# Kernel optimization log

Hardware: AMD Instinct MI355X
Metric: run time of the kernel (lower is better)

## Reference

```python
import jax, jax.numpy as jnp
import numpy as np

ALPHA = 0.1
B, T, D = 32, 1024, 384


def _build_alive(T):
    # Expert j (1-indexed) is created at time j with lifetime 2^(ctz(j)+2)+1.
    def lifetime(j):
        k = (j & -j).bit_length() - 1
        return 2 ** (k + 2) + 1

    sets = [[j for j in range(1, t + 1) if t < j + lifetime(j)]
            for t in range(1, T + 1)]
    K = max(len(s) for s in sets)
    # pad with sentinel index T (the extra never-consumed expert slot)
    idx = np.full((T, K), T, dtype=np.int32)
    mask = np.zeros((T, K), dtype=np.float32)
    for t0, s in enumerate(sets):
        for i, j in enumerate(s):
            idx[t0, i] = j - 1  # 0-indexed expert slot
            mask[t0, i] = 1.0
    return idx, mask


def setup_inputs() -> dict:
    key = jax.random.key(0)
    kx, kw, kb = jax.random.split(key, 3)
    n_exp = T + 1
    x = jax.random.normal(kx, (B, T, D), dtype=jnp.float32)
    # stand-in STULayer = Linear(D, D) per expert
    W = jax.random.normal(kw, (n_exp, D, D), dtype=jnp.float32) / np.float32(np.sqrt(D))
    b = jax.random.normal(kb, (n_exp, D), dtype=jnp.float32) * 0.02
    idx, mask = _build_alive(T)
    return {"x": x, "W": W, "b": b,
            "alive_idx": jnp.asarray(idx), "alive_mask": jnp.asarray(mask)}


def reference(x, W, b, alive_idx, alive_mask):
    Bb, Tt, Dd = x.shape
    n_exp = W.shape[0]
    # initial pool: 1 expert with weight 1
    p0 = jnp.zeros((n_exp,), x.dtype).at[0].set(1.0)
    new_idx = jnp.arange(1, Tt + 1, dtype=jnp.int32)      # slot of expert created at step t
    t_f = jnp.arange(1, Tt + 1, dtype=x.dtype)            # p[new] = 1/t

    def step(p, inp):
        x_t, idx, mask, ni, tf = inp          # x_t: [B,D]; idx,mask: [K]
        Wg = W[idx]                            # [K,D,D]
        bg = b[idx]                            # [K,D]
        outs = jnp.einsum('bd,kde->kbe', x_t, Wg) + bg[:, None, :]  # [K,B,D]
        p_a = p[idx] * mask                    # weights of alive experts
        w = p_a / jnp.sum(p_a)                 # normalized (torch keeps them pre-normalized)
        y_t = jnp.einsum('k,kbe->be', w, outs)
        # soft cross-entropy of expert outputs against x_t (ChunkedCrossEntropyLoss stand-in)
        tgt = jax.nn.softmax(x_t, axis=-1)                       # [B,D]
        logp = jax.nn.log_softmax(outs, axis=-1)                 # [K,B,D]
        loss = -jnp.mean(jnp.sum(tgt[None, :, :] * logp, axis=-1), axis=-1)  # [K]
        loss = jax.lax.stop_gradient(loss)     # torch uses .item() => detached
        # multiplicative weight update, normalize over alive set
        p_upd = p_a * jnp.exp(-ALPHA * loss) * mask
        p_upd = p_upd / jnp.sum(p_upd)
        p = p.at[idx].set(jnp.where(mask > 0, p_upd, p[idx]))
        # spawn new expert with weight 1/t (renormalization deferred to use time)
        p = p.at[ni].set(1.0 / tf)
        return p, y_t

    xs = (jnp.swapaxes(x, 0, 1), alive_idx, alive_mask, new_idx, t_f)
    _, ys = jax.lax.scan(step, p0, xs)        # ys: [T,B,D]
    return jnp.swapaxes(ys, 0, 1)
```

## Files before the change

### kernel.cpp

```cpp
#include <hip/hip_runtime.h>

#define TT 1024
#define BB 32
#define DD 384
#define NE 1025
#define ALPHA_ 0.1f
#define TC 4
#define KSTEP 64
#define NKS 6
#define MROWS 128
#define PADK 72
#define NTHR 512

typedef __attribute__((ext_vector_type(8))) short short8;
typedef __attribute__((ext_vector_type(8))) unsigned short ushort8;
typedef __attribute__((ext_vector_type(4))) float f32x4;

__device__ __forceinline__ unsigned short f2bf(float f) {
    unsigned int u = __float_as_uint(f);
    unsigned int r = u + 0x7fffu + ((u >> 16) & 1u);
    return (unsigned short)(r >> 16);
}

__device__ __host__ __forceinline__ int chunks_of(int j, int* Lout) {
    int k = __builtin_ctz(j);
    int life = (1 << (k + 2)) + 1;
    int jend = j + life - 1; if (jend > TT) jend = TT;
    int L = jend - j + 1;
    *Lout = L;
    return (L + TC - 1) / TC;
}

__device__ __forceinline__ void gl16(const void* g, void* l) {
    __builtin_amdgcn_global_load_lds(
        (const __attribute__((address_space(1))) void*)g,
        (__attribute__((address_space(3))) void*)l, 16, 0, 0);
}

__device__ __forceinline__ float dppsum32(float v) {
    float t;
    t = __int_as_float(__builtin_amdgcn_update_dpp(0, __float_as_int(v), 0x111, 0xf, 0xf, true)); v += t;
    t = __int_as_float(__builtin_amdgcn_update_dpp(0, __float_as_int(v), 0x112, 0xf, 0xf, true)); v += t;
    t = __int_as_float(__builtin_amdgcn_update_dpp(0, __float_as_int(v), 0x114, 0xf, 0xf, true)); v += t;
    t = __int_as_float(__builtin_amdgcn_update_dpp(0, __float_as_int(v), 0x118, 0xf, 0xf, true)); v += t;
    t = __int_as_float(__builtin_amdgcn_update_dpp(0, __float_as_int(v), 0x142, 0xf, 0xf, true)); v += t;
    return __int_as_float(__builtin_amdgcn_readlane(__float_as_int(v), 31));
}

__global__ void setup_blocks(int* __restrict__ table) {
    int j = threadIdx.x + 1;
    int L; int nc = chunks_of(j, &L);
    int start = 0;
    for (int jp = 1; jp < j; ++jp) { int Lp; start += chunks_of(jp, &Lp); }
    for (int c = 0; c < nc; ++c) {
        int cnt = L - c * TC; if (cnt > TC) cnt = TC;
        int* e = table + 3 * (start + c);
        e[0] = j - 1;
        e[1] = (j - 1) + c * TC;
        e[2] = cnt;
    }
}

__global__ void setup_pref(const float* __restrict__ amask, int* __restrict__ pref, int K) {
    __shared__ int sc[1024];
    int t = threadIdx.x;
    int c = 0;
    for (int kk = 0; kk < K; ++kk) c += (amask[t * K + kk] > 0.f) ? 1 : 0;
    sc[t] = c;
    __syncthreads();
    for (int off = 1; off < 1024; off <<= 1) {
        int v = (t >= off) ? sc[t - off] : 0;
        __syncthreads();
        sc[t] += v;
        __syncthreads();
    }
    if (t == 0) pref[0] = 0;
    pref[t + 1] = sc[t];
}

__global__ void setup_union(int* __restrict__ uCount, int* __restrict__ uList) {
    int c = threadIdx.x;
    int t1 = 2 * c + 1, t2 = 2 * c + 2;
    int n = 0;
    for (int j = 1; j <= t2 && j <= TT; ++j) {
        int k = __builtin_ctz(j);
        int life = (1 << (k + 2)) + 1;
        if (j + life - 1 >= t1) { if (n < 32) uList[c * 32 + n] = j - 1; n++; }
    }
    uCount[c] = n > 32 ? 32 : n;
}

__global__ void setup_perm3(const int* __restrict__ aidx, const float* __restrict__ amask,
                            short* __restrict__ perm16, int K) {
    int t0 = blockIdx.x;
    int l = threadIdx.x;
    short enc = 63;
    if (t0 >= 1 && t0 <= TT - 1 && l < K && amask[t0 * K + l] > 0.f) {
        int sp = aidx[t0 * K + l];
        if (sp == t0) enc = (short)(-sp);
        else {
            for (int kk = 0; kk < K; ++kk)
                if (aidx[(t0 - 1) * K + kk] == sp) { enc = (short)kk; break; }
        }
    }
    perm16[t0 * 32 + l] = enc;
}

__global__ void conv_w(const float* __restrict__ W, unsigned short* __restrict__ Wperm) {
    int db = blockIdx.x;
    int j  = blockIdx.y;
    __shared__ __align__(16) unsigned short sL[12288];
    int tid = threadIdx.x;
    int r = tid >> 4, q = tid & 15;
    const float* src = W + (size_t)j * (DD * DD) + (size_t)(db * 32 + r) * DD + q * 24;
#pragma unroll
    for (int i = 0; i < 6; ++i) {
        float4 f = *(const float4*)(src + i * 4);
        int e0 = q * 24 + i * 4;
        float fv[4] = {f.x, f.y, f.z, f.w};
#pragma unroll
        for (int m = 0; m < 4; ++m) {
            int e = e0 + m;
            int off = (e >> 4) * 512 + (r >> 3) * 128 + (e & 15) * 8 + (r & 7);
            sL[off] = f2bf(fv[m]);
        }
    }
    __syncthreads();
    ushort8* dst = (ushort8*)(Wperm + ((size_t)j * 12 + db) * 12288);
    const ushort8* s8 = (const ushort8*)sL;
#pragma unroll
    for (int i = 0; i < 3; ++i) dst[tid * 3 + i] = s8[tid * 3 + i];
}

__global__ void conv_x(const float* __restrict__ x, unsigned short* __restrict__ xperm) {
    int t = blockIdx.x;
    __shared__ __align__(16) unsigned short sL[12288];
    int tid = threadIdx.x;
    int b = tid >> 4, q = tid & 15;
    const float* src = x + ((size_t)b * TT + t) * DD + q * 24;
#pragma unroll
    for (int i = 0; i < 6; ++i) {
        float4 f = *(const float4*)(src + i * 4);
        int d0 = q * 24 + i * 4;
        float fv[4] = {f.x, f.y, f.z, f.w};
#pragma unroll
        for (int m = 0; m < 4; ++m) {
            int d = d0 + m;
            int off = ((b >> 4) * 12 + (d >> 5)) * 512 + ((d >> 3) & 3) * 128 + (b & 15) * 8 + (d & 7);
            sL[off] = f2bf(fv[m]);
        }
    }
    __syncthreads();
    ushort8* dst = (ushort8*)(xperm + (size_t)t * 12288);
    const ushort8* s8 = (const ushort8*)sL;
#pragma unroll
    for (int i = 0; i < 3; ++i) dst[tid * 3 + i] = s8[tid * 3 + i];
}

__global__ void conv_tgt(const float* __restrict__ x, unsigned short* __restrict__ tgtbf) {
    __shared__ unsigned short sL[8 * 384];
    int tid = threadIdx.x;
    int wid = tid >> 6, lane = tid & 63;
    size_t row = (size_t)blockIdx.x * 8 + wid;
    const float* xr = x + row * DD;
    float v[6]; float m = -1e30f;
#pragma unroll
    for (int i = 0; i < 6; ++i) { v[i] = xr[lane + 64 * i]; m = fmaxf(m, v[i]); }
#pragma unroll
    for (int d = 1; d < 64; d <<= 1) m = fmaxf(m, __shfl_xor(m, d));
    float s = 0.f;
#pragma unroll
    for (int i = 0; i < 6; ++i) { v[i] = __expf(v[i] - m); s += v[i]; }
#pragma unroll
    for (int d = 1; d < 64; d <<= 1) s += __shfl_xor(s, d);
    float rz = 1.0f / s;
#pragma unroll
    for (int i = 0; i < 6; ++i) sL[wid * 384 + lane + 64 * i] = f2bf(v[i] * rz);
    __syncthreads();
    unsigned int* dst = (unsigned int*)(tgtbf + (size_t)blockIdx.x * 8 * 384);
    const unsigned int* s32 = (const unsigned int*)sL;
#pragma unroll
    for (int i = 0; i < 3; ++i) dst[tid * 3 + i] = s32[tid * 3 + i];
}

__global__ __launch_bounds__(1024)
void gemmA(const unsigned short* __restrict__ xperm,
           const unsigned short* __restrict__ Wperm,
           const float* __restrict__ bias,
           const int* __restrict__ aidx,
           const unsigned short* __restrict__ tgtbf,
           float* __restrict__ Epad,
           const int* __restrict__ table, int nblk, int K,
           const int* __restrict__ pref,
           unsigned short* __restrict__ outs)
{
    __shared__ __align__(16) unsigned short sA[2][4096];
    __shared__ __align__(16) unsigned short sB[2][12288];
    __shared__ float sRow[128];
    __shared__ int sKK[TC];
    __shared__ int sSlot[TC];

    int bid = blockIdx.x;
    int q8 = nblk >> 3, r8 = nblk & 7;
    int xcd = bid & 7, pos = bid >> 3;
    int lb = (xcd < r8 ? xcd * (q8 + 1) : r8 * (q8 + 1) + (xcd - r8) * q8) + pos;

    int s = table[3 * lb], t0s = table[3 * lb + 1], cnt = table[3 * lb + 2];

    int tid = threadIdx.x;
    int wid = tid >> 6, lane = tid & 63;
    int waveM = wid >> 2, waveN = wid & 3;
    int lc = lane & 15, lg = lane >> 4;

    int tcl[4];
#pragma unroll
    for (int tc = 0; tc < 4; ++tc) { int t = t0s + tc; tcl[tc] = t > TT - 1 ? TT - 1 : t; }

    f32x4 acc[2][6];
    f32x4 zz = {0.f, 0.f, 0.f, 0.f};
#pragma unroll
    for (int m = 0; m < 2; ++m)
#pragma unroll
        for (int n = 0; n < 6; ++n) acc[m][n] = zz;

    const size_t wbase = (size_t)s * (12 * 24 * 512);

    auto stage = [&](int buf, int ks) {
        if (wid < 8) {
            int tc = wid >> 1, bb = wid & 1;
            const unsigned short* asrc = xperm + ((size_t)tcl[tc] * 24 + bb * 12 + ks) * 512 + lane * 8;
            gl16(asrc, &sA[buf][wid * 512]);
            const unsigned short* bsrc = Wperm + wbase + ((size_t)ks * 24 + 16 + wid) * 512 + lane * 8;
            gl16(bsrc, &sB[buf][(16 + wid) * 512]);
        } else {
            int e0 = (wid - 8) * 2;
            const unsigned short* b0 = Wperm + wbase + ((size_t)ks * 24 + e0) * 512 + lane * 8;
            gl16(b0, &sB[buf][e0 * 512]);
            gl16(b0 + 512, &sB[buf][(e0 + 1) * 512]);
        }
    };

    stage(0, 0);
    __syncthreads();
    for (int ks = 0; ks < 12; ++ks) {
        int cur = ks & 1;
        if (ks < 11) stage(cur ^ 1, ks + 1);
        short8 af[2], bfr[6];
#pragma unroll
        for (int mf = 0; mf < 2; ++mf)
            af[mf] = *(const short8*)&sA[cur][(waveM * 2 + mf) * 512 + lane * 8];
#pragma unroll
        for (int nf = 0; nf < 6; ++nf)
            bfr[nf] = *(const short8*)&sB[cur][(waveN * 6 + nf) * 512 + lane * 8];
#pragma unroll
        for (int mf = 0; mf < 2; ++mf)
#pragma unroll
            for (int nf = 0; nf < 6; ++nf)
                acc[mf][nf] = __builtin_amdgcn_mfma_f32_16x16x32_bf16(af[mf], bfr[nf], acc[mf][nf], 0, 0, 0);
        __syncthreads();
    }

    float* sStat = (float*)&sA[0][0];
    if (tid < TC) {
        int kk = 0, slot = 0;
        if (tid < cnt) {
            int t = t0s + tid;
            for (int k2 = 0; k2 < K; ++k2)
                if (aidx[t * K + k2] == s) { kk = k2; break; }
            if (pref) slot = pref[t] + kk;
        }
        sKK[tid] = kk;
        sSlot[tid] = slot;
    }
#pragma unroll
    for (int nf = 0; nf < 6; ++nf) {
        float be = bias[(size_t)s * DD + waveN * 96 + nf * 16 + lc];
#pragma unroll
        for (int mf = 0; mf < 2; ++mf)
#pragma unroll
            for (int rr = 0; rr < 4; ++rr) acc[mf][nf][rr] += be;
    }
#pragma unroll
    for (int mf = 0; mf < 2; ++mf)
#pragma unroll
        for (int rr = 0; rr < 4; ++rr) {
            float m = acc[mf][0][rr];
#pragma unroll
            for (int nf = 1; nf < 6; ++nf) m = fmaxf(m, acc[mf][nf][rr]);
#pragma unroll
            for (int d = 1; d < 16; d <<= 1) m = fmaxf(m, __shfl_xor(m, d));
            if (lc == 0) sStat[(waveM * 32 + mf * 16 + lg * 4 + rr) * 12 + waveN] = m;
        }
    __syncthreads();
    if (outs && waveM < cnt) {
        unsigned short* ob = outs + (size_t)sSlot[waveM] * 12288;
#pragma unroll
        for (int mf = 0; mf < 2; ++mf)
#pragma unroll
            for (int nf = 0; nf < 6; ++nf) {
                int e = waveN * 96 + nf * 16 + lc;
#pragma unroll
                for (int rr = 0; rr < 4; ++rr) {
                    int b = mf * 16 + lg * 4 + rr;
                    ob[b * 384 + e] = f2bf(acc[mf][nf][rr]);
                }
            }
    }
#pragma unroll
    for (int mf = 0; mf < 2; ++mf)
#pragma unroll
        for (int rr = 0; rr < 4; ++rr) {
            int row = waveM * 32 + mf * 16 + lg * 4 + rr;
            const f32x4 pm = *(const f32x4*)&sStat[row * 12];
            float rmax = fmaxf(fmaxf(pm[0], pm[1]), fmaxf(pm[2], pm[3]));
            int tcr = row >> 5, b = row & 31;
            int t = tcl[tcr];
            const unsigned short* tg = tgtbf + ((size_t)b * TT + t) * DD;
            float psum = 0.f, pdot = 0.f;
#pragma unroll
            for (int nf = 0; nf < 6; ++nf) {
                int e = waveN * 96 + nf * 16 + lc;
                float a = acc[mf][nf][rr];
                psum += __expf(a - rmax);
                float tv = __uint_as_float(((unsigned int)tg[e]) << 16);
                pdot += tv * a;
            }
#pragma unroll
            for (int d = 1; d < 16; d <<= 1) { psum += __shfl_xor(psum, d); pdot += __shfl_xor(pdot, d); }
            if (lc == 0) { sStat[row * 12 + 4 + waveN] = psum; sStat[row * 12 + 8 + waveN] = pdot; }
        }
    __syncthreads();
    if (wid == 0) {
#pragma unroll
        for (int h = 0; h < 2; ++h) {
            int row = lane + h * 64;
            const f32x4 mm = *(const f32x4*)&sStat[row * 12];
            const f32x4 pp = *(const f32x4*)&sStat[row * 12 + 4];
            const f32x4 dd = *(const f32x4*)&sStat[row * 12 + 8];
            float rmax = fmaxf(fmaxf(mm[0], mm[1]), fmaxf(mm[2], mm[3]));
            float S = pp[0] + pp[1] + pp[2] + pp[3];
            float Dt = dd[0] + dd[1] + dd[2] + dd[3];
            sRow[row] = rmax + logf(S) - Dt;
        }
    }
    __syncthreads();
    if (wid == 0) {
#pragma unroll
        for (int pph = 0; pph < 2; ++pph) {
            int tc = pph * 2 + (lane >> 5);
            int b = lane & 31;
            float v = (tc < cnt) ? sRow[tc * 32 + b] : 0.f;
#pragma unroll
            for (int d = 1; d < 32; d <<= 1) v += __shfl_xor(v, d);
            if (b == 0 && tc < cnt) {
                float loss = v * (1.0f / 32.0f);
                float E = expf(-ALPHA_ * loss);
                int t0 = t0s + tc;
                Epad[t0 * 32 + sKK[tc]] = E;
            }
        }
    }
}

__global__ __launch_bounds__(256)
void recur3(const float* __restrict__ Epad, const short* __restrict__ perm16,
            const int* __restrict__ aidx, const float* __restrict__ amask,
            float* __restrict__ wraw, int K) {
    __shared__ __align__(16) float sE[2][4096];
    __shared__ __align__(16) short sP[2][4160];
    int tid = threadIdx.x, wid = tid >> 6, lane = tid & 63;
    int l = lane;

    auto stageCh = [&](int buf, int c) {
        const float* eb = Epad + c * 4096;
#pragma unroll
        for (int i = wid; i < 16; i += 4)
            gl16(eb + i * 256 + lane * 4, &sE[buf][i * 256]);
        const short* pb = perm16 + (c * 128 + 1) * 32;
#pragma unroll
        for (int i = wid; i < 8; i += 4)
            gl16(pb + i * 512 + lane * 8, &sP[buf][32 + i * 512]);
    };

    stageCh(0, 0);
    __syncthreads();

    float pr = 0.f;
    if (l < K && amask[l] > 0.f && aidx[l] == 0) pr = 1.f;

    int buf = 0;
    for (int c = 0; c < 8; ++c) {
        if (c < 7) stageCh(buf ^ 1, c + 1);
        if (wid == 0) {
            float curE = (l < 32) ? sE[buf][l] : 0.f;
            short curP = (l < 32) ? sP[buf][32 + l] : (short)63;
            for (int tl = 0; tl < 128; ++tl) {
                float nE = 0.f; short nP = 63;
                if (tl < 127) {
                    nE = sE[buf][(tl + 1) * 32 + (l & 31)];
                    nP = sP[buf][(tl + 2) * 32 + (l & 31)];
                }
                int t = c * 128 + tl;
                if (l < 32) wraw[t * 32 + l] = pr;
                float qv = pr * curE;
                float S2 = dppsum32(qv);
                float pn = qv / S2;
                int pe = (l < 32) ? (int)curP : 63;
                int src = pe >= 0 ? pe : 0;
                float sv = __shfl(pn, src);
                pr = (pe >= 0) ? sv : (1.0f / (float)(-pe));
                curE = (l < 32) ? nE : 0.f;
                curP = nP;
            }
        }
        __syncthreads();
        buf ^= 1;
    }
}

__global__ void wnorm(float* __restrict__ w) {
    int tid = threadIdx.x;
    int wid = tid >> 6, lane = tid & 63;
    int half = lane >> 5, l = lane & 31;
    int t = blockIdx.x * 8 + wid * 2 + half;
    float v = w[t * 32 + l];
    float s = v;
#pragma unroll
    for (int d = 1; d < 32; d <<= 1) s += __shfl_xor(s, d);
    w[t * 32 + l] = v / s;
}

__global__ __launch_bounds__(512)
void mixout(const unsigned short* __restrict__ outs, const float* __restrict__ wts32,
            const int* __restrict__ pref, float* __restrict__ y) {
    int t = blockIdx.x;
    __shared__ float sW[32];
    int tid = threadIdx.x;
    if (tid < 32) sW[tid] = wts32[t * 32 + tid];
    __syncthreads();
    int p0 = pref[t];
    int L = pref[t + 1] - p0;
    float acc[24];
#pragma unroll
    for (int i = 0; i < 24; ++i) acc[i] = 0.f;
    const ushort8* base = (const ushort8*)(outs + (size_t)p0 * 12288);
    for (int kk = 0; kk < L; ++kk) {
        float w = sW[kk];
        const ushort8* sp = base + (size_t)kk * 1536;
#pragma unroll
        for (int pass = 0; pass < 3; ++pass) {
            ushort8 v = sp[pass * 512 + tid];
#pragma unroll
            for (int j = 0; j < 8; ++j)
                acc[pass * 8 + j] += w * __uint_as_float(((unsigned int)v[j]) << 16);
        }
    }
#pragma unroll
    for (int pass = 0; pass < 3; ++pass) {
        int c = pass * 512 + tid;
        int b = c / 48;
        int e = (c % 48) * 8;
        float* yr = y + ((size_t)b * TT + t) * DD + e;
        float4 f0, f1;
        f0.x = acc[pass * 8 + 0]; f0.y = acc[pass * 8 + 1];
        f0.z = acc[pass * 8 + 2]; f0.w = acc[pass * 8 + 3];
        f1.x = acc[pass * 8 + 4]; f1.y = acc[pass * 8 + 5];
        f1.z = acc[pass * 8 + 6]; f1.w = acc[pass * 8 + 7];
        *(float4*)yr = f0;
        *(float4*)(yr + 4) = f1;
    }
}

__global__ __launch_bounds__(1024)
void gemmC(const unsigned short* __restrict__ xperm,
           const unsigned short* __restrict__ Wperm,
           const float* __restrict__ bias,
           const int* __restrict__ aidx,
           const float* __restrict__ wts32,
           const int* __restrict__ uCount, const int* __restrict__ uList,
           float* __restrict__ y, int K)
{
    __shared__ __align__(16) unsigned short sAF[24576];
    __shared__ __align__(16) unsigned short sB[2][12288];
    __shared__ float sWu[64];
    __shared__ int   sUL[32];
    __shared__ float sBv[768];

    int nb = gridDim.x;
    int bid = blockIdx.x;
    int q8 = nb >> 3, r8 = nb & 7;
    int xcd = bid & 7, pos = bid >> 3;
    int c = (xcd < r8 ? xcd * (q8 + 1) : r8 * (q8 + 1) + (xcd - r8) * q8) + pos;

    int t0 = c * 2;
    int tid = threadIdx.x, wid = tid >> 6, lane = tid & 63;
    int waveM = wid >> 2, waveN = wid & 3;
    int lc = lane & 15, lg = lane >> 4;
    int tcw = waveM >> 1, bbw = waveM & 1;

    int uc = uCount[c];
    if (tid < uc) sUL[tid] = uList[c * 32 + tid];
#pragma unroll
    for (int i = 0; i < 3; ++i) {
        int T = wid * 3 + i;
        int tc = T / 24, bb = (T / 12) & 1, db = T % 12;
        const unsigned short* src = xperm + ((size_t)(t0 + tc) * 24 + bb * 12 + db) * 512 + lane * 8;
        gl16(src, &sAF[T * 512]);
    }
    __syncthreads();
    if (tid < 2 * uc) {
        int u = tid >> 1, tc = tid & 1;
        int j = sUL[u];
        float wv = 0.f;
        for (int kk = 0; kk < K; ++kk)
            if (aidx[(t0 + tc) * K + kk] == j) { wv = wts32[(t0 + tc) * 32 + kk]; break; }
        sWu[u * 2 + tc] = wv;
    }
    __syncthreads();
    {
        size_t wb = (size_t)sUL[0] * (12 * 24 * 512);
        const unsigned short* b0 = Wperm + wb + (size_t)wid * 512 + lane * 8;
        gl16(b0, &sB[0][wid * 512]);
        if (wid < 8) {
            const unsigned short* b1 = Wperm + wb + (size_t)(16 + wid) * 512 + lane * 8;
            gl16(b1, &sB[0][(16 + wid) * 512]);
        }
    }
    for (int i = tid; i < 768; i += 1024) {
        int tc = (i >= 384) ? 1 : 0; int e = i - tc * 384;
        float a = 0.f;
        for (int u = 0; u < uc; ++u) a += sWu[u * 2 + tc] * bias[(size_t)sUL[u] * DD + e];
        sBv[i] = a;
    }
    __syncthreads();

    f32x4 accY[6], accE[6];
    f32x4 zz = {0.f, 0.f, 0.f, 0.f};
#pragma unroll
    for (int n = 0; n < 6; ++n) { accY[n] = zz; accE[n] = zz; }

    int buf = 0;
    for (int u = 0; u < uc; ++u) {
        float wv = sWu[u * 2 + tcw];
        bool act = (wv != 0.f);
        for (int ks = 0; ks < 12; ++ks) {
            int nu = u, nk = ks + 1;
            if (nk == 12) { nk = 0; nu = u + 1; }
            if (nu < uc) {
                size_t wb = (size_t)sUL[nu] * (12 * 24 * 512) + (size_t)nk * (24 * 512);
                const unsigned short* b0 = Wperm + wb + (size_t)wid * 512 + lane * 8;
                gl16(b0, &sB[buf ^ 1][wid * 512]);
                if (wid < 8) {
                    const unsigned short* b1 = Wperm + wb + (size_t)(16 + wid) * 512 + lane * 8;
                    gl16(b1, &sB[buf ^ 1][(16 + wid) * 512]);
                }
            }
            if (act) {
                short8 af = *(const short8*)&sAF[(waveM * 12 + ks) * 512 + lane * 8];
#pragma unroll
                for (int nf = 0; nf < 6; ++nf) {
                    short8 bf = *(const short8*)&sB[buf][(waveN * 6 + nf) * 512 + lane * 8];
                    accE[nf] = __builtin_amdgcn_mfma_f32_16x16x32_bf16(af, bf, accE[nf], 0, 0, 0);
                }
            }
            __syncthreads();
            buf ^= 1;
        }
        if (act) {
#pragma unroll
            for (int nf = 0; nf < 6; ++nf)
#pragma unroll
                for (int rr = 0; rr < 4; ++rr) { accY[nf][rr] += wv * accE[nf][rr]; accE[nf][rr] = 0.f; }
        }
    }

    int t = t0 + tcw;
#pragma unroll
    for (int nf = 0; nf < 6; ++nf) {
        int e = waveN * 96 + nf * 16 + lc;
        float bvv = sBv[tcw * 384 + e];
#pragma unroll
        for (int rr = 0; rr < 4; ++rr) {
            int b = bbw * 16 + lg * 4 + rr;
            y[((size_t)b * TT + t) * DD + e] = accY[nf][rr] + bvv;
        }
    }
}

__global__ void rowstats(const float* __restrict__ x, float* __restrict__ xm,
                         float* __restrict__ rz) {
    int wid = threadIdx.x >> 6;
    int lane = threadIdx.x & 63;
    int row = blockIdx.x * 4 + wid;
    const float* xr = x + (size_t)row * DD;
    float v[6];
    float m = -1e30f;
#pragma unroll
    for (int i = 0; i < 6; ++i) { v[i] = xr[lane + 64 * i]; m = fmaxf(m, v[i]); }
#pragma unroll
    for (int d = 1; d < 64; d <<= 1) m = fmaxf(m, __shfl_xor(m, d));
    float s = 0.f;
#pragma unroll
    for (int i = 0; i < 6; ++i) s += expf(v[i] - m);
#pragma unroll
    for (int d = 1; d < 64; d <<= 1) s += __shfl_xor(s, d);
    if (lane == 0) { xm[row] = m; rz[row] = 1.0f / s; }
}

template<int MODE>
__global__ __launch_bounds__(NTHR)
void gemm_phase(const float* __restrict__ x, const float* __restrict__ W,
                const float* __restrict__ bias, const int* __restrict__ aidx,
                const float* __restrict__ xm, const float* __restrict__ rz,
                const float* __restrict__ wts, float* __restrict__ Earr,
                float* __restrict__ y, const int* __restrict__ table,
                int nblk, int K)
{
    __shared__ __align__(16) unsigned short sA[MROWS * PADK];
    __shared__ __align__(16) unsigned short sB[DD * PADK];
    __shared__ float sRow[MROWS];
    __shared__ float sCoef[TC];

    int bid = blockIdx.x;
    int q = nblk >> 3, r = nblk & 7;
    int xcd = bid & 7, pos = bid >> 3;
    int lb = (xcd < r ? xcd * (q + 1) : r * (q + 1) + (xcd - r) * q) + pos;

    int s = table[3 * lb], t0s = table[3 * lb + 1], cnt = table[3 * lb + 2];

    int tid = threadIdx.x;
    int wid = tid >> 6, lane = tid & 63;
    int waveM = wid >> 2, waveN = wid & 3;
    int lc = lane & 15, lg = lane >> 4;

    if (MODE == 1 && tid < TC) {
        float c = 0.f;
        if (tid < cnt) {
            int t0 = t0s + tid;
            for (int kk = 0; kk < K; ++kk)
                if (aidx[t0 * K + kk] == s) { c = wts[t0 * K + kk]; break; }
        }
        sCoef[tid] = c;
    }

    f32x4 acc[4][6];
    f32x4 zz = {0.f, 0.f, 0.f, 0.f};
#pragma unroll
    for (int i = 0; i < 4; ++i)
#pragma unroll
        for (int n = 0; n < 6; ++n) acc[i][n] = zz;

    const float* Wj = W + (size_t)s * (DD * DD);

    int xr = tid >> 2, xq = tid & 3;
    int xtc = xr >> 5, xb = xr & 31;
    int xt = t0s + xtc; if (xt > TT - 1) xt = TT - 1;
    const float* xrow = x + ((size_t)xb * TT + xt) * DD;

    for (int ks = 0; ks < NKS; ++ks) {
        const int d0 = ks * KSTEP;
        __syncthreads();
        {
            const float4* src = (const float4*)(xrow + d0 + xq * 16);
            float4 f0 = src[0], f1 = src[1], f2 = src[2], f3 = src[3];
            short8 v0, v1;
            v0[0] = (short)f2bf(f0.x); v0[1] = (short)f2bf(f0.y);
            v0[2] = (short)f2bf(f0.z); v0[3] = (short)f2bf(f0.w);
            v0[4] = (short)f2bf(f1.x); v0[5] = (short)f2bf(f1.y);
            v0[6] = (short)f2bf(f1.z); v0[7] = (short)f2bf(f1.w);
            v1[0] = (short)f2bf(f2.x); v1[1] = (short)f2bf(f2.y);
            v1[2] = (short)f2bf(f2.z); v1[3] = (short)f2bf(f2.w);
            v1[4] = (short)f2bf(f3.x); v1[5] = (short)f2bf(f3.y);
            v1[6] = (short)f2bf(f3.z); v1[7] = (short)f2bf(f3.w);
            short8* dst = (short8*)&sA[xr * PADK + xq * 16];
            dst[0] = v0; dst[1] = v1;
        }
        {
            int dbase = d0 + wid * 8;
#pragma unroll
            for (int g = 0; g < 6; ++g) {
                int e = g * 64 + lane;
                const float* col = Wj + (size_t)dbase * DD + e;
                short8 h;
#pragma unroll
                for (int dd = 0; dd < 8; ++dd) h[dd] = (short)f2bf(col[(size_t)dd * DD]);
                *(short8*)&sB[e * PADK + wid * 8] = h;
            }
        }
        __syncthreads();
#pragma unroll
        for (int kh = 0; kh < 2; ++kh) {
            short8 af[4], bfr[6];
#pragma unroll
            for (int mf = 0; mf < 4; ++mf)
                af[mf] = *(const short8*)&sA[(waveM * 64 + mf * 16 + lc) * PADK + kh * 32 + lg * 8];
#pragma unroll
            for (int nf = 0; nf < 6; ++nf)
                bfr[nf] = *(const short8*)&sB[(waveN * 96 + nf * 16 + lc) * PADK + kh * 32 + lg * 8];
#pragma unroll
            for (int mf = 0; mf < 4; ++mf)
#pragma unroll
                for (int nf = 0; nf < 6; ++nf)
                    acc[mf][nf] = __builtin_amdgcn_mfma_f32_16x16x32_bf16(af[mf], bfr[nf], acc[mf][nf], 0, 0, 0);
        }
    }

    if (MODE == 0) {
        __syncthreads();
        float* sStat = (float*)sA;
#pragma unroll
        for (int nf = 0; nf < 6; ++nf) {
            float be = bias[(size_t)s * DD + waveN * 96 + nf * 16 + lc];
#pragma unroll
            for (int mf = 0; mf < 4; ++mf)
#pragma unroll
                for (int rr = 0; rr < 4; ++rr) acc[mf][nf][rr] += be;
        }
#pragma unroll
        for (int mf = 0; mf < 4; ++mf)
#pragma unroll
            for (int rr = 0; rr < 4; ++rr) {
                float m = acc[mf][0][rr];
#pragma unroll
                for (int nf = 1; nf < 6; ++nf) m = fmaxf(m, acc[mf][nf][rr]);
#pragma unroll
                for (int d = 1; d < 16; d <<= 1) m = fmaxf(m, __shfl_xor(m, d));
                if (lc == 0) sStat[(waveM * 64 + mf * 16 + lg * 4 + rr) * 12 + waveN] = m;
            }
        __syncthreads();
#pragma unroll
        for (int mf = 0; mf < 4; ++mf)
#pragma unroll
            for (int rr = 0; rr < 4; ++rr) {
                int row = waveM * 64 + mf * 16 + lg * 4 + rr;
                const f32x4 pm = *(const f32x4*)&sStat[row * 12];
                float rmax = fmaxf(fmaxf(pm[0], pm[1]), fmaxf(pm[2], pm[3]));
                int tc = row >> 5, b = row & 31;
                int t = t0s + tc; if (t > TT - 1) t = TT - 1;
                float xmv = xm[b * TT + t];
                float rzv = rz[b * TT + t];
                const float* x2 = x + ((size_t)b * TT + t) * DD;
                float psum = 0.f, pdot = 0.f;
#pragma unroll
                for (int nf = 0; nf < 6; ++nf) {
                    int e = waveN * 96 + nf * 16 + lc;
                    float a = acc[mf][nf][rr];
                    psum += __expf(a - rmax);
                    float tg = __expf(x2[e] - xmv) * rzv;
                    pdot += tg * a;
                }
#pragma unroll
                for (int d = 1; d < 16; d <<= 1) {
                    psum += __shfl_xor(psum, d);
                    pdot += __shfl_xor(pdot, d);
                }
                if (lc == 0) { sStat[row * 12 + 4 + waveN] = psum; sStat[row * 12 + 8 + waveN] = pdot; }
            }
        __syncthreads();
        if (wid == 0) {
#pragma unroll
            for (int h = 0; h < 2; ++h) {
                int row = lane + h * 64;
                const f32x4 mm = *(const f32x4*)&sStat[row * 12];
                const f32x4 pp = *(const f32x4*)&sStat[row * 12 + 4];
                const f32x4 dd = *(const f32x4*)&sStat[row * 12 + 8];
                float rmax = fmaxf(fmaxf(mm[0], mm[1]), fmaxf(mm[2], mm[3]));
                float S = pp[0] + pp[1] + pp[2] + pp[3];
                float Dt = dd[0] + dd[1] + dd[2] + dd[3];
                sRow[row] = rmax + logf(S) - Dt;
            }
        }
        __syncthreads();
        if (wid == 0) {
#pragma unroll
            for (int pph = 0; pph < 2; ++pph) {
                int tc = pph * 2 + (lane >> 5);
                int b = lane & 31;
                float v = (tc < cnt) ? sRow[tc * 32 + b] : 0.f;
#pragma unroll
                for (int d = 1; d < 32; d <<= 1) v += __shfl_xor(v, d);
                if (b == 0 && tc < cnt) {
                    float loss = v * (1.0f / 32.0f);
                    float E = expf(-ALPHA_ * loss);
                    int t0 = t0s + tc;
                    for (int kk = 0; kk < K; ++kk)
                        if (aidx[t0 * K + kk] == s) { Earr[t0 * K + kk] = E; break; }
                }
            }
        }
    } else {
#pragma unroll
        for (int mf = 0; mf < 4; ++mf)
#pragma unroll
            for (int rr = 0; rr < 4; ++rr) {
                int row = waveM * 64 + mf * 16 + lg * 4 + rr;
                int tc = row >> 5, b = row & 31;
                if (tc < cnt) {
                    float c = sCoef[tc];
                    int t = t0s + tc;
                    float* yr = y + ((size_t)b * TT + t) * DD + waveN * 96 + lc;
#pragma unroll
                    for (int nf = 0; nf < 6; ++nf)
                        atomicAdd(yr + nf * 16, c * acc[mf][nf][rr]);
                }
            }
    }
}

__global__ void recurrence(const int* __restrict__ aidx, const float* __restrict__ amask,
                           const float* __restrict__ Earr, float* __restrict__ wts, int K) {
    __shared__ float p[NE];
    int l = threadIdx.x;
    for (int i = l; i < NE; i += 64) p[i] = 0.f;
    __syncthreads();
    if (l == 0) p[0] = 1.f;
    __syncthreads();

    int idxv = TT; float mv = 0.f, Ev = 1.f;
    if (l < K) { idxv = aidx[l]; mv = amask[l]; Ev = Earr[l]; }

    for (int t0 = 0; t0 < TT; ++t0) {
        int idxn = TT; float mn = 0.f, En = 1.f;
        if (t0 + 1 < TT && l < K) {
            idxn = aidx[(t0 + 1) * K + l];
            mn = amask[(t0 + 1) * K + l];
            En = Earr[(t0 + 1) * K + l];
        }
        float pa = (l < K) ? p[idxv] * mv : 0.f;
        float qv = pa * Ev;
        float S1 = pa, S2 = qv;
#pragma unroll
        for (int d = 1; d < 64; d <<= 1) {
            S1 += __shfl_xor(S1, d);
            S2 += __shfl_xor(S2, d);
        }
        float w = pa / S1;
        if (l < K) wts[t0 * K + l] = w;
        float pn = qv / S2;
        __syncthreads();
        if (l < K && mv > 0.f) p[idxv] = pn;
        if (l == 0) p[t0 + 1] = 1.0f / (float)(t0 + 1);
        __syncthreads();
        idxv = idxn; mv = mn; Ev = En;
    }
}

__global__ void bias_init(const float* __restrict__ bias, const int* __restrict__ aidx,
                          const float* __restrict__ wts, float* __restrict__ y, int K) {
    int t0 = blockIdx.x;
    int e = threadIdx.x;
    float acc = 0.f;
    for (int kk = 0; kk < K; ++kk) {
        float w = wts[t0 * K + kk];
        int s = aidx[t0 * K + kk];
        acc += w * bias[(size_t)s * DD + e];
    }
    for (int b = 0; b < BB; ++b)
        y[((size_t)b * TT + t0) * DD + e] = acc;
}

extern "C" void kernel_launch(void* const* d_in, const int* in_sizes, int n_in,
                              void* d_out, int out_size, void* d_ws, size_t ws_size,
                              hipStream_t stream) {
    const float* x = (const float*)d_in[0];
    const float* W = (const float*)d_in[1];
    const float* bv = (const float*)d_in[2];
    const int* aidx = (const int*)d_in[3];
    const float* amask = (const float*)d_in[4];
    float* y = (float*)d_out;
    const int K = in_sizes[3] / TT;

    int nblk = 0, NSLOT = 0;
    for (int j = 1; j <= TT; ++j) { int L; nblk += chunks_of(j, &L); NSLOT += L; }

    size_t szW = (size_t)1024 * 294912;
    size_t szX = (size_t)1024 * 24576;
    size_t szT = (size_t)BB * TT * DD * 2;
    size_t szEp = (size_t)TT * 32 * sizeof(float);
    size_t szWt = (size_t)TT * 32 * sizeof(float);
    size_t szPm = (size_t)(TT + 1) * 32 * sizeof(short);
    size_t szTab = (size_t)6144 * 3 * sizeof(int);
    size_t szUC = 512 * sizeof(int);
    size_t szUL = 512 * 32 * sizeof(int);
    size_t szO  = (size_t)NSLOT * 12288 * 2;
    size_t szPf = (size_t)(TT + 1) * sizeof(int);
    size_t need2 = szW + szX + szT + szEp + szWt + szPm + szTab + szUC + szUL + 256;
    size_t need1 = need2 + szO + szPf;

    if (ws_size >= need1) {
        unsigned char* p = (unsigned char*)d_ws;
        unsigned short* Wperm = (unsigned short*)p; p += szW;
        unsigned short* xperm = (unsigned short*)p; p += szX;
        unsigned short* tgtb  = (unsigned short*)p; p += szT;
        float* Epad = (float*)p; p += szEp;
        float* wts32 = (float*)p; p += szWt;
        short* perm16 = (short*)p; p += szPm;
        int* table  = (int*)p;   p += szTab;
        int* uCnt   = (int*)p;   p += szUC;
        int* uLst   = (int*)p;   p += szUL;
        int* pref   = (int*)p;   p += szPf;
        unsigned short* outs = (unsigned short*)p; p += szO;

        hipLaunchKernelGGL(setup_blocks, dim3(1), dim3(1024), 0, stream, table);
        hipLaunchKernelGGL(setup_pref, dim3(1), dim3(1024), 0, stream, amask, pref, K);
        hipLaunchKernelGGL(setup_perm3, dim3(TT + 1), dim3(32), 0, stream, aidx, amask, perm16, K);
        hipLaunchKernelGGL(conv_w, dim3(12, 1024), dim3(512), 0, stream, W, Wperm);
        hipLaunchKernelGGL(conv_x, dim3(TT), dim3(512), 0, stream, x, xperm);
        hipLaunchKernelGGL(conv_tgt, dim3(BB * TT / 8), dim3(512), 0, stream, x, tgtb);
        hipMemsetAsync(Epad, 0, szEp, stream);
        hipLaunchKernelGGL(gemmA, dim3(nblk), dim3(1024), 0, stream,
                           xperm, Wperm, bv, aidx, tgtb, Epad, table, nblk, K, pref, outs);
        hipLaunchKernelGGL(recur3, dim3(1), dim3(256), 0, stream,
                           Epad, perm16, aidx, amask, wts32, K);
        hipLaunchKernelGGL(wnorm, dim3(TT / 8), dim3(256), 0, stream, wts32);
        hipLaunchKernelGGL(mixout, dim3(TT), dim3(512), 0, stream, outs, wts32, pref, y);
    } else if (ws_size >= need2) {
        unsigned char* p = (unsigned char*)d_ws;
        unsigned short* Wperm = (unsigned short*)p; p += szW;
        unsigned short* xperm = (unsigned short*)p; p += szX;
        unsigned short* tgtb  = (unsigned short*)p; p += szT;
        float* Epad = (float*)p; p += szEp;
        float* wts32 = (float*)p; p += szWt;
        short* perm16 = (short*)p; p += szPm;
        int* table  = (int*)p;   p += szTab;
        int* uCnt   = (int*)p;   p += szUC;
        int* uLst   = (int*)p;   p += szUL;

        hipLaunchKernelGGL(setup_blocks, dim3(1), dim3(1024), 0, stream, table);
        hipLaunchKernelGGL(setup_union, dim3(1), dim3(512), 0, stream, uCnt, uLst);
        hipLaunchKernelGGL(setup_perm3, dim3(TT + 1), dim3(32), 0, stream, aidx, amask, perm16, K);
        hipLaunchKernelGGL(conv_w, dim3(12, 1024), dim3(512), 0, stream, W, Wperm);
        hipLaunchKernelGGL(conv_x, dim3(TT), dim3(512), 0, stream, x, xperm);
        hipLaunchKernelGGL(conv_tgt, dim3(BB * TT / 8), dim3(512), 0, stream, x, tgtb);
        hipMemsetAsync(Epad, 0, szEp, stream);
        hipLaunchKernelGGL(gemmA, dim3(nblk), dim3(1024), 0, stream,
                           xperm, Wperm, bv, aidx, tgtb, Epad, table, nblk, K,
                           (const int*)nullptr, (unsigned short*)nullptr);
        hipLaunchKernelGGL(recur3, dim3(1), dim3(256), 0, stream,
                           Epad, perm16, aidx, amask, wts32, K);
        hipLaunchKernelGGL(wnorm, dim3(TT / 8), dim3(256), 0, stream, wts32);
        hipLaunchKernelGGL(gemmC, dim3(512), dim3(1024), 0, stream,
                           xperm, Wperm, bv, aidx, wts32, uCnt, uLst, y, K);
    } else {
        float* Earr = (float*)d_ws;
        float* wts = Earr + (size_t)TT * K;
        float* xm = wts + (size_t)TT * K;
        float* rz = xm + (size_t)BB * TT;
        int* table = (int*)(rz + (size_t)BB * TT);

        hipLaunchKernelGGL(setup_blocks, dim3(1), dim3(1024), 0, stream, table);
        hipLaunchKernelGGL(rowstats, dim3(BB * TT / 4), dim3(256), 0, stream, x, xm, rz);
        hipLaunchKernelGGL((gemm_phase<0>), dim3(nblk), dim3(NTHR), 0, stream,
                           x, W, bv, aidx, xm, rz, (const float*)nullptr, Earr,
                           (float*)nullptr, table, nblk, K);
        hipLaunchKernelGGL(recurrence, dim3(1), dim3(64), 0, stream, aidx, amask, Earr, wts, K);
        hipLaunchKernelGGL(bias_init, dim3(TT), dim3(DD), 0, stream, bv, aidx, wts, y, K);
        hipLaunchKernelGGL((gemm_phase<1>), dim3(nblk), dim3(NTHR), 0, stream,
                           x, W, bv, aidx, xm, rz, wts, (float*)nullptr, y, table, nblk, K);
    }
}
```

Baseline: 1.088 ms.

## Merge setup kernels, drop LDS staging in conversions, deepen gemmA prefetch pipeline

Three setup kernels are merged into one launch that branches on block index. The W and x bf16 conversion kernels now write the permuted layout straight from registers instead of staging through shared memory. conv_tgt's final copy is changed to coalesced strided stores. gemmA gets a two-stage-ahead prefetch controlled by explicit vmcnt waits and raw barriers, plus a launch_bounds occupancy hint. These target launch overhead, LDS traffic and load latency in the GEMM, at the cost of strided global reads in conv_w2 and a more fragile manual synchronisation scheme.

```diff
diff --git a/kernel.cpp b/kernel.cpp
--- a/kernel.cpp
+++ b/kernel.cpp
@@ -47,114 +47,90 @@
     return __int_as_float(__builtin_amdgcn_readlane(__float_as_int(v), 31));
 }
 
-__global__ void setup_blocks(int* __restrict__ table) {
-    int j = threadIdx.x + 1;
-    int L; int nc = chunks_of(j, &L);
-    int start = 0;
-    for (int jp = 1; jp < j; ++jp) { int Lp; start += chunks_of(jp, &Lp); }
-    for (int c = 0; c < nc; ++c) {
-        int cnt = L - c * TC; if (cnt > TC) cnt = TC;
-        int* e = table + 3 * (start + c);
-        e[0] = j - 1;
-        e[1] = (j - 1) + c * TC;
-        e[2] = cnt;
-    }
-}
-
-__global__ void setup_pref(const float* __restrict__ amask, int* __restrict__ pref, int K) {
+__global__ void setup_all(int* __restrict__ table, int* __restrict__ pref,
+                          short* __restrict__ perm16,
+                          const int* __restrict__ aidx, const float* __restrict__ amask,
+                          int K) {
     __shared__ int sc[1024];
-    int t = threadIdx.x;
-    int c = 0;
-    for (int kk = 0; kk < K; ++kk) c += (amask[t * K + kk] > 0.f) ? 1 : 0;
-    sc[t] = c;
-    __syncthreads();
-    for (int off = 1; off < 1024; off <<= 1) {
-        int v = (t >= off) ? sc[t - off] : 0;
+    int b = blockIdx.x, t = threadIdx.x;
+    if (b == 0) {
+        int j = t + 1;
+        int L; int nc = chunks_of(j, &L);
+        int start = 0;
+        for (int jp = 1; jp < j; ++jp) { int Lp; start += chunks_of(jp, &Lp); }
+        for (int c = 0; c < nc; ++c) {
+            int cnt = L - c * TC; if (cnt > TC) cnt = TC;
+            int* e = table + 3 * (start + c);
+            e[0] = j - 1;
+            e[1] = (j - 1) + c * TC;
+            e[2] = cnt;
+        }
+    } else if (b == 1) {
+        int c = 0;
+        for (int kk = 0; kk < K; ++kk) c += (amask[t * K + kk] > 0.f) ? 1 : 0;
+        sc[t] = c;
         __syncthreads();
-        sc[t] += v;
-        __syncthreads();
-    }
-    if (t == 0) pref[0] = 0;
-    pref[t + 1] = sc[t];
-}
-
-__global__ void setup_union(int* __restrict__ uCount, int* __restrict__ uList) {
-    int c = threadIdx.x;
-    int t1 = 2 * c + 1, t2 = 2 * c + 2;
-    int n = 0;
-    for (int j = 1; j <= t2 && j <= TT; ++j) {
-        int k = __builtin_ctz(j);
-        int life = (1 << (k + 2)) + 1;
-        if (j + life - 1 >= t1) { if (n < 32) uList[c * 32 + n] = j - 1; n++; }
-    }
-    uCount[c] = n > 32 ? 32 : n;
-}
-
-__global__ void setup_perm3(const int* __restrict__ aidx, const float* __restrict__ amask,
-                            short* __restrict__ perm16, int K) {
-    int t0 = blockIdx.x;
-    int l = threadIdx.x;
-    short enc = 63;
-    if (t0 >= 1 && t0 <= TT - 1 && l < K && amask[t0 * K + l] > 0.f) {
-        int sp = aidx[t0 * K + l];
-        if (sp == t0) enc = (short)(-sp);
-        else {
-            for (int kk = 0; kk < K; ++kk)
-                if (aidx[(t0 - 1) * K + kk] == sp) { enc = (short)kk; break; }
-        }
-    }
-    perm16[t0 * 32 + l] = enc;
-}
-
-__global__ void conv_w(const float* __restrict__ W, unsigned short* __restrict__ Wperm) {
+        for (int off = 1; off < 1024; off <<= 1) {
+            int v = (t >= off) ? sc[t - off] : 0;
+            __syncthreads();
+            sc[t] += v;
+            __syncthreads();
+        }
+        if (t == 0) pref[0] = 0;
+        pref[t + 1] = sc[t];
+    } else {
+        int t0 = b - 2;
+        int l = t;
+        if (l < 32) {
+            short enc = 63;
+            if (t0 >= 1 && t0 <= TT - 1 && l < K && amask[t0 * K + l] > 0.f) {
+                int sp = aidx[t0 * K + l];
+                if (sp == t0) enc = (short)(-sp);
+                else {
+                    for (int kk = 0; kk < K; ++kk)
+                        if (aidx[(t0 - 1) * K + kk] == sp) { enc = (short)kk; break; }
+                }
+            }
+            perm16[t0 * 32 + l] = enc;
+        }
+    }
+}
+
+__global__ __launch_bounds__(512)
+void conv_w2(const float* __restrict__ W, unsigned short* __restrict__ Wperm) {
     int db = blockIdx.x;
     int j  = blockIdx.y;
-    __shared__ __align__(16) unsigned short sL[12288];
-    int tid = threadIdx.x;
-    int r = tid >> 4, q = tid & 15;
-    const float* src = W + (size_t)j * (DD * DD) + (size_t)(db * 32 + r) * DD + q * 24;
-#pragma unroll
-    for (int i = 0; i < 6; ++i) {
-        float4 f = *(const float4*)(src + i * 4);
-        int e0 = q * 24 + i * 4;
-        float fv[4] = {f.x, f.y, f.z, f.w};
-#pragma unroll
-        for (int m = 0; m < 4; ++m) {
-            int e = e0 + m;
-            int off = (e >> 4) * 512 + (r >> 3) * 128 + (e & 15) * 8 + (r & 7);
-            sL[off] = f2bf(fv[m]);
-        }
-    }
-    __syncthreads();
-    ushort8* dst = (ushort8*)(Wperm + ((size_t)j * 12 + db) * 12288);
-    const ushort8* s8 = (const ushort8*)sL;
-#pragma unroll
-    for (int i = 0; i < 3; ++i) dst[tid * 3 + i] = s8[tid * 3 + i];
-}
-
-__global__ void conv_x(const float* __restrict__ x, unsigned short* __restrict__ xperm) {
+    int tid = threadIdx.x, l = tid & 63, w8 = tid >> 6;
+    const float* Wj = W + (size_t)j * (DD * DD)
+                        + (size_t)(db * 32 + (l >> 4) * 8) * DD + (l & 15);
+#pragma unroll
+    for (int it = 0; it < 3; ++it) {
+        int eblk = it * 8 + w8;
+        const float* src = Wj + eblk * 16;
+        ushort8 h;
+#pragma unroll
+        for (int k = 0; k < 8; ++k) h[k] = f2bf(src[(size_t)k * DD]);
+        *(ushort8*)&Wperm[(((size_t)j * 12 + db) * 24 + eblk) * 512 + l * 8] = h;
+    }
+}
+
+__global__ __launch_bounds__(512)
+void conv_x2(const float* __restrict__ x, unsigned short* __restrict__ xperm) {
     int t = blockIdx.x;
-    __shared__ __align__(16) unsigned short sL[12288];
-    int tid = threadIdx.x;
-    int b = tid >> 4, q = tid & 15;
-    const float* src = x + ((size_t)b * TT + t) * DD + q * 24;
-#pragma unroll
-    for (int i = 0; i < 6; ++i) {
-        float4 f = *(const float4*)(src + i * 4);
-        int d0 = q * 24 + i * 4;
-        float fv[4] = {f.x, f.y, f.z, f.w};
-#pragma unroll
-        for (int m = 0; m < 4; ++m) {
-            int d = d0 + m;
-            int off = ((b >> 4) * 12 + (d >> 5)) * 512 + ((d >> 3) & 3) * 128 + (b & 15) * 8 + (d & 7);
-            sL[off] = f2bf(fv[m]);
-        }
-    }
-    __syncthreads();
-    ushort8* dst = (ushort8*)(xperm + (size_t)t * 12288);
-    const ushort8* s8 = (const ushort8*)sL;
-#pragma unroll
-    for (int i = 0; i < 3; ++i) dst[tid * 3 + i] = s8[tid * 3 + i];
+    int tid = threadIdx.x, l = tid & 63, w8 = tid >> 6;
+#pragma unroll
+    for (int it = 0; it < 3; ++it) {
+        int T = it * 8 + w8;
+        int bb = T / 12, db = T - bb * 12;
+        const float* src = x + ((size_t)(bb * 16 + (l & 15)) * TT + t) * DD
+                             + db * 32 + (l >> 4) * 8;
+        float4 f0 = *(const float4*)src;
+        float4 f1 = *(const float4*)(src + 4);
+        ushort8 h;
+        h[0] = f2bf(f0.x); h[1] = f2bf(f0.y); h[2] = f2bf(f0.z); h[3] = f2bf(f0.w);
+        h[4] = f2bf(f1.x); h[5] = f2bf(f1.y); h[6] = f2bf(f1.z); h[7] = f2bf(f1.w);
+        *(ushort8*)&xperm[(size_t)t * 12288 + T * 512 + l * 8] = h;
+    }
 }
 
 __global__ void conv_tgt(const float* __restrict__ x, unsigned short* __restrict__ tgtbf) {
@@ -180,10 +156,10 @@
     unsigned int* dst = (unsigned int*)(tgtbf + (size_t)blockIdx.x * 8 * 384);
     const unsigned int* s32 = (const unsigned int*)sL;
 #pragma unroll
-    for (int i = 0; i < 3; ++i) dst[tid * 3 + i] = s32[tid * 3 + i];
-}
-
-__global__ __launch_bounds__(1024)
+    for (int i = 0; i < 3; ++i) dst[i * 512 + tid] = s32[i * 512 + tid];
+}
+
+__global__ __launch_bounds__(1024, 8)
 void gemmA(const unsigned short* __restrict__ xperm,
            const unsigned short* __restrict__ Wperm,
            const float* __restrict__ bias,
@@ -241,10 +217,13 @@
     };
 
     stage(0, 0);
-    __syncthreads();
+    stage(1, 1);
     for (int ks = 0; ks < 12; ++ks) {
         int cur = ks & 1;
-        if (ks < 11) stage(cur ^ 1, ks + 1);
+        if (ks < 11) asm volatile("s_waitcnt vmcnt(2)" ::: "memory");
+        else         asm volatile("s_waitcnt vmcnt(0)" ::: "memory");
+        __builtin_amdgcn_s_barrier();
+        __builtin_amdgcn_sched_barrier(0);
         short8 af[2], bfr[6];
 #pragma unroll
         for (int mf = 0; mf < 2; ++mf)
@@ -257,8 +236,12 @@
 #pragma unroll
             for (int nf = 0; nf < 6; ++nf)
                 acc[mf][nf] = __builtin_amdgcn_mfma_f32_16x16x32_bf16(af[mf], bfr[nf], acc[mf][nf], 0, 0, 0);
-        __syncthreads();
-    }
+        __builtin_amdgcn_sched_barrier(0);
+        __builtin_amdgcn_s_barrier();
+        __builtin_amdgcn_sched_barrier(0);
+        if (ks < 10) stage(cur, ks + 2);
+    }
+    __syncthreads();
 
     float* sStat = (float*)&sA[0][0];
     if (tid < TC) {
@@ -471,6 +454,99 @@
     }
 }
 
+__global__ void setup_blocks(int* __restrict__ table) {
+    int j = threadIdx.x + 1;
+    int L; int nc = chunks_of(j, &L);
+    int start = 0;
+    for (int jp = 1; jp < j; ++jp) { int Lp; start += chunks_of(jp, &Lp); }
+    for (int c = 0; c < nc; ++c) {
+        int cnt = L - c * TC; if (cnt > TC) cnt = TC;
+        int* e = table + 3 * (start + c);
+        e[0] = j - 1;
+        e[1] = (j - 1) + c * TC;
+        e[2] = cnt;
+    }
+}
+
+__global__ void setup_union(int* __restrict__ uCount, int* __restrict__ uList) {
+    int c = threadIdx.x;
+    int t1 = 2 * c + 1, t2 = 2 * c + 2;
+    int n = 0;
+    for (int j = 1; j <= t2 && j <= TT; ++j) {
+        int k = __builtin_ctz(j);
+        int life = (1 << (k + 2)) + 1;
+        if (j + life - 1 >= t1) { if (n < 32) uList[c * 32 + n] = j - 1; n++; }
+    }
+    uCount[c] = n > 32 ? 32 : n;
+}
+
+__global__ void setup_perm3(const int* __restrict__ aidx, const float* __restrict__ amask,
+                            short* __restrict__ perm16, int K) {
+    int t0 = blockIdx.x;
+    int l = threadIdx.x;
+    short enc = 63;
+    if (t0 >= 1 && t0 <= TT - 1 && l < K && amask[t0 * K + l] > 0.f) {
+        int sp = aidx[t0 * K + l];
+        if (sp == t0) enc = (short)(-sp);
+        else {
+            for (int kk = 0; kk < K; ++kk)
+                if (aidx[(t0 - 1) * K + kk] == sp) { enc = (short)kk; break; }
+        }
+    }
+    perm16[t0 * 32 + l] = enc;
+}
+
+__global__ void conv_w(const float* __restrict__ W, unsigned short* __restrict__ Wperm) {
+    int db = blockIdx.x;
+    int j  = blockIdx.y;
+    __shared__ __align__(16) unsigned short sL[12288];
+    int tid = threadIdx.x;
+    int r = tid >> 4, q = tid & 15;
+    const float* src = W + (size_t)j * (DD * DD) + (size_t)(db * 32 + r) * DD + q * 24;
+#pragma unroll
+    for (int i = 0; i < 6; ++i) {
+        float4 f = *(const float4*)(src + i * 4);
+        int e0 = q * 24 + i * 4;
+        float fv[4] = {f.x, f.y, f.z, f.w};
+#pragma unroll
+        for (int m = 0; m < 4; ++m) {
+            int e = e0 + m;
+            int off = (e >> 4) * 512 + (r >> 3) * 128 + (e & 15) * 8 + (r & 7);
+            sL[off] = f2bf(fv[m]);
+        }
+    }
+    __syncthreads();
+    ushort8* dst = (ushort8*)(Wperm + ((size_t)j * 12 + db) * 12288);
+    const ushort8* s8 = (const ushort8*)sL;
+#pragma unroll
+    for (int i = 0; i < 3; ++i) dst[tid * 3 + i] = s8[tid * 3 + i];
+}
+
+__global__ void conv_x(const float* __restrict__ x, unsigned short* __restrict__ xperm) {
+    int t = blockIdx.x;
+    __shared__ __align__(16) unsigned short sL[12288];
+    int tid = threadIdx.x;
+    int b = tid >> 4, q = tid & 15;
+    const float* src = x + ((size_t)b * TT + t) * DD + q * 24;
+#pragma unroll
+    for (int i = 0; i < 6; ++i) {
+        float4 f = *(const float4*)(src + i * 4);
+        int d0 = q * 24 + i * 4;
+        float fv[4] = {f.x, f.y, f.z, f.w};
+#pragma unroll
+        for (int m = 0; m < 4; ++m) {
+            int d = d0 + m;
+            int off = ((b >> 4) * 12 + (d >> 5)) * 512 + ((d >> 3) & 3) * 128 + (b & 15) * 8 + (d & 7);
+            sL[off] = f2bf(fv[m]);
+        }
+    }
+    __syncthreads();
+    ushort8* dst = (ushort8*)(xperm + (size_t)t * 12288);
+    const ushort8* s8 = (const ushort8*)sL;
+#pragma unroll
+    for (int i = 0; i < 3; ++i) dst[tid * 3 + i] = s8[tid * 3 + i];
+}
+
 __global__ __launch_bounds__(1024)
 void gemmC(const unsigned short* __restrict__ xperm,
            const unsigned short* __restrict__ Wperm,
@@ -901,11 +977,10 @@
         int* pref   = (int*)p;   p += szPf;
         unsigned short* outs = (unsigned short*)p; p += szO;
 
-        hipLaunchKernelGGL(setup_blocks, dim3(1), dim3(1024), 0, stream, table);
-        hipLaunchKernelGGL(setup_pref, dim3(1), dim3(1024), 0, stream, amask, pref, K);
-        hipLaunchKernelGGL(setup_perm3, dim3(TT + 1), dim3(32), 0, stream, aidx, amask, perm16, K);
-        hipLaunchKernelGGL(conv_w, dim3(12, 1024), dim3(512), 0, stream, W, Wperm);
-        hipLaunchKernelGGL(conv_x, dim3(TT), dim3(512), 0, stream, x, xperm);
+        hipLaunchKernelGGL(setup_all, dim3(TT + 3), dim3(1024), 0, stream,
+                           table, pref, perm16, aidx, amask, K);
+        hipLaunchKernelGGL(conv_w2, dim3(12, 1024), dim3(512), 0, stream, W, Wperm);
+        hipLaunchKernelGGL(conv_x2, dim3(TT), dim3(512), 0, stream, x, xperm);
         hipLaunchKernelGGL(conv_tgt, dim3(BB * TT / 8), dim3(512), 0, stream, x, tgtb);
         hipMemsetAsync(Epad, 0, szEp, stream);
         hipLaunchKernelGGL(gemmA, dim3(nblk), dim3(1024), 0, stream,
```

Measured after the change: 3.142 ms. 2.89x slower.
